# Kernel tuning notes

Measured on AMD Instinct MI355X. Metric: run time of the kernel, lower is better.

Reference implementation:

```python
import jax, jax.numpy as jnp
import numpy as np

B, T, CIN, F, K, U, FF, N, LS = 16, 384, 64, 64, 32, 128, 1024, 64, 15
EPS = 1e-3  # keras BatchNormalization epsilon

def _conv1d(x, w):
    # x:[B,T,C], w:[K,C,F], 'same' padding, no bias
    return jax.lax.conv_general_dilated(x, w, (1,), 'SAME', dimension_numbers=('NWC', 'WIO', 'NWC'))

def _bn(x, g, b, m, v):
    # inference-mode batchnorm
    return g * (x - m) * jax.lax.rsqrt(v + EPS) + b

def _gru_seq(x, k, rk, b):
    # keras GRU (reset_after=True), gate order [z, r, h]; x:[B,T,D] -> [B,T,U]
    u = rk.shape[0]
    xp = x @ k + b[0]                      # precompute input projections [B,T,3U]
    def step(h, xt):
        rec = h @ rk + b[1]
        xz, xr, xh = jnp.split(xt, 3, axis=-1)
        rz, rr_, rh = jnp.split(rec, 3, axis=-1)
        z = jax.nn.sigmoid(xz + rz)
        r = jax.nn.sigmoid(xr + rr_)
        hh = jnp.tanh(xh + r * rh)
        hn = z * h + (1.0 - z) * hh
        return hn, hn
    h0 = jnp.zeros((x.shape[0], u), x.dtype)
    _, ys = jax.lax.scan(step, h0, jnp.swapaxes(xp, 0, 1))
    return jnp.swapaxes(ys, 0, 1)

def _cgru(xr, xi, kr, rkr, br, ki, rki, bi):
    # ComplexGRUCell: real_gru applied to both parts, imag_gru applied to both parts
    rr = _gru_seq(xr, kr, rkr, br)
    ri = _gru_seq(xi, kr, rkr, br)
    ir = _gru_seq(xr, ki, rki, bi)
    ii = _gru_seq(xi, ki, rki, bi)
    return rr - ii, ri + ir

def _forward(h_real, h_imag, conv_wr, conv_wi, bn_gr, bn_br, bn_mr, bn_vr, bn_gi, bn_bi, bn_mi, bn_vi, g0_kr, g0_rkr, g0_br, g0_ki, g0_rki, g0_bi, gs_kr, gs_rkr, gs_br, gs_ki, gs_rki, gs_bi, ff1_w, ff1_b, ff2_w, ff2_b, qr_w, qr_b, qi_w, qi_b, rr_w, rr_b, ri_w, ri_b):
    xr = _bn(_conv1d(h_real, conv_wr) - _conv1d(h_imag, conv_wi), bn_gr, bn_br, bn_mr, bn_vr)
    xi = _bn(_conv1d(h_imag, conv_wr) + _conv1d(h_real, conv_wi), bn_gi, bn_bi, bn_mi, bn_vi)
    xr, xi = _cgru(xr, xi, g0_kr, g0_rkr, g0_br, g0_ki, g0_rki, g0_bi)
    for i in range(LS):  # fixed small layer count
        xr, xi = _cgru(xr, xi, gs_kr[i], gs_rkr[i], gs_br[i], gs_ki[i], gs_rki[i], gs_bi[i])
    def ff(a):
        return jax.nn.relu(a @ ff1_w + ff1_b) @ ff2_w + ff2_b
    xr = xr + ff(xr)   # dropout is identity at inference
    xi = xi + ff(xi)
    mr = jnp.mean(xr, axis=1)
    mi = jnp.mean(xi, axis=1)
    Qr = (mr @ qr_w + qr_b) - (mi @ qi_w + qi_b)
    Qi = (mi @ qr_w + qr_b) + (mr @ qi_w + qi_b)
    Rr = (mr @ rr_w + rr_b) - (mi @ ri_w + ri_b)
    Ri = (mi @ rr_w + rr_b) + (mr @ ri_w + ri_b)
    Qr = Qr.reshape(-1, N, N); Qi = Qi.reshape(-1, N, N)
    Rr = Rr.reshape(-1, N, N); Ri = Ri.reshape(-1, N, N)
    # trace(Q Q^H) = sum |Q|^2 (real, nonnegative)
    nrm = jnp.sqrt(jnp.sum(Qr * Qr + Qi * Qi, axis=(1, 2)))[:, None, None]
    scale = jnp.sqrt(jnp.float32(N)) / nrm
    return Qr * scale, Qi * scale, Rr, Ri

def setup_inputs():
    key = jax.random.key(0)
    ks = jax.random.split(key, 20)
    s = 0.05
    def nrm(k, shape, scale=s):
        return jax.random.normal(k, shape, jnp.float32) * scale
    inp = {}
    inp['h_real'] = nrm(ks[0], (B, T, CIN), 1.0)
    inp['h_imag'] = nrm(ks[1], (B, T, CIN), 1.0)
    inp['conv_wr'] = nrm(ks[2], (K, CIN, F))
    inp['conv_wi'] = nrm(ks[3], (K, CIN, F))
    for nm in ('bn_gr', 'bn_gi', 'bn_vr', 'bn_vi'):
        inp[nm] = jnp.ones((F,), jnp.float32)
    for nm in ('bn_br', 'bn_bi', 'bn_mr', 'bn_mi'):
        inp[nm] = jnp.zeros((F,), jnp.float32)
    inp['g0_kr'] = nrm(ks[4], (F, 3 * U));  inp['g0_rkr'] = nrm(ks[5], (U, 3 * U));  inp['g0_br'] = jnp.zeros((2, 3 * U), jnp.float32)
    inp['g0_ki'] = nrm(ks[6], (F, 3 * U));  inp['g0_rki'] = nrm(ks[7], (U, 3 * U));  inp['g0_bi'] = jnp.zeros((2, 3 * U), jnp.float32)
    inp['gs_kr'] = nrm(ks[8], (LS, U, 3 * U));  inp['gs_rkr'] = nrm(ks[9], (LS, U, 3 * U));  inp['gs_br'] = jnp.zeros((LS, 2, 3 * U), jnp.float32)
    inp['gs_ki'] = nrm(ks[10], (LS, U, 3 * U)); inp['gs_rki'] = nrm(ks[11], (LS, U, 3 * U)); inp['gs_bi'] = jnp.zeros((LS, 2, 3 * U), jnp.float32)
    inp['ff1_w'] = nrm(ks[12], (U, FF)); inp['ff1_b'] = jnp.zeros((FF,), jnp.float32)
    inp['ff2_w'] = nrm(ks[13], (FF, U)); inp['ff2_b'] = jnp.zeros((U,), jnp.float32)
    inp['qr_w'] = nrm(ks[14], (U, N * N)); inp['qr_b'] = jnp.zeros((N * N,), jnp.float32)
    inp['qi_w'] = nrm(ks[15], (U, N * N)); inp['qi_b'] = jnp.zeros((N * N,), jnp.float32)
    inp['rr_w'] = nrm(ks[16], (U, N * N)); inp['rr_b'] = jnp.zeros((N * N,), jnp.float32)
    inp['ri_w'] = nrm(ks[17], (U, N * N)); inp['ri_b'] = jnp.zeros((N * N,), jnp.float32)
    return inp

def reference(h_real, h_imag, conv_wr, conv_wi, bn_gr, bn_br, bn_mr, bn_vr, bn_gi, bn_bi, bn_mi, bn_vi, g0_kr, g0_rkr, g0_br, g0_ki, g0_rki, g0_bi, gs_kr, gs_rkr, gs_br, gs_ki, gs_rki, gs_bi, ff1_w, ff1_b, ff2_w, ff2_b, qr_w, qr_b, qi_w, qi_b, rr_w, rr_b, ri_w, ri_b):
    return _forward(h_real, h_imag, conv_wr, conv_wi, bn_gr, bn_br, bn_mr, bn_vr, bn_gi, bn_bi, bn_mi, bn_vi, g0_kr, g0_rkr, g0_br, g0_ki, g0_rki, g0_bi, gs_kr, gs_rkr, gs_br, gs_ki, gs_rki, gs_bi, ff1_w, ff1_b, ff2_w, ff2_b, qr_w, qr_b, qi_w, qi_b, rr_w, rr_b, ri_w, ri_b)
```

## Files before the change

### kernel.cpp

```cpp
#include <hip/hip_runtime.h>
#include <hip/hip_bf16.h>
#include <math.h>

typedef __attribute__((ext_vector_type(8))) short short8;
typedef __attribute__((ext_vector_type(4))) float f32x4;
typedef unsigned short u16;
typedef unsigned int u32;

#define CL 16
#define NCHUNK 24
#define RING 4
#define CHSZ (16*CL*128)

__device__ __forceinline__ u16 f2bf(float f){
  u32 x = __float_as_uint(f);
  u32 r = x + 0x7fffu + ((x >> 16) & 1u);
  return (u16)(r >> 16);
}
__device__ __forceinline__ float bf2f(u16 u){
  return __uint_as_float(((u32)u) << 16);
}
__device__ __forceinline__ f32x4 mfma16(short8 a, short8 b, f32x4 c){
  return __builtin_amdgcn_mfma_f32_16x16x32_bf16(a, b, c, 0, 0, 0);
}

__global__ void k_init(float* S, float* ssq, u32* Flg){
  int i = blockIdx.x*256 + threadIdx.x;
  if (i < 32768){ S[i] = 0.f; return; }
  i -= 32768;
  if (i < 16){ ssq[i] = 0.f; return; }
  i -= 16;
  if (i < 4096){ Flg[i] = 0u; return; }
}

__global__ void k_wprep(const float* __restrict__ wr, const float* __restrict__ wi,
                        const float* __restrict__ w1,
                        u16* WtR, u16* WtI, u16* WtIN, u16* W1t){
  int i = blockIdx.x*256 + threadIdx.x;
  if (i < 131072){
    int k = i >> 12, r = i & 4095, f = r >> 6, c = r & 63;
    float a = wr[(k<<12) + (c<<6) + f];
    float b = wi[(k<<12) + (c<<6) + f];
    WtR[i] = f2bf(a); WtI[i] = f2bf(b); WtIN[i] = f2bf(-b);
  } else if (i < 262144){
    int j = i - 131072;
    int col = j >> 7, k = j & 127;
    W1t[j] = f2bf(w1[(k<<10) + col]);
  }
}

__global__ __launch_bounds__(256) void k_wprep2(
    const float* __restrict__ g0_kr, const float* __restrict__ g0_ki,
    const float* __restrict__ gs_kr, const float* __restrict__ gs_ki,
    const float* __restrict__ g0_rkr, const float* __restrict__ g0_rki,
    const float* __restrict__ gs_rkr, const float* __restrict__ gs_rki,
    u16* __restrict__ KT, u16* __restrict__ RKT){
  __shared__ float tile[128][33];
  int bid = blockIdx.x;
  int ct = bid % 12; int lm = (bid/12) & 31; int which = bid / (12*32);
  int m = lm & 1, l = lm >> 1;
  int c0 = ct*32;
  int tid = threadIdx.x;
  for (int idx = tid; idx < 128*32; idx += 256){
    int k = idx >> 5, cc = idx & 31;
    float v;
    if (!which){
      if (l == 0) v = (k < 64) ? (m ? g0_ki : g0_kr)[k*384 + c0+cc] : 0.f;
      else        v = (m ? gs_ki : gs_kr)[((size_t)(l-1)*128 + k)*384 + c0+cc];
    } else {
      if (l == 0) v = (m ? g0_rki : g0_rkr)[k*384 + c0+cc];
      else        v = (m ? gs_rki : gs_rkr)[((size_t)(l-1)*128 + k)*384 + c0+cc];
    }
    tile[k][cc] = v;
  }
  __syncthreads();
  u16* dst = (which ? RKT : KT) + (size_t)lm*384*128;
  for (int idx = tid; idx < 32*128; idx += 256){
    int cc = idx >> 7, k = idx & 127;
    dst[(size_t)(c0+cc)*128 + k] = f2bf(tile[k][cc]);
  }
}

__global__ __launch_bounds__(256) void k_conv(
    const float* __restrict__ hr, const float* __restrict__ hi,
    const u16* __restrict__ WtR, const u16* __restrict__ WtI, const u16* __restrict__ WtIN,
    const float* __restrict__ gr, const float* __restrict__ gi,
    const float* __restrict__ vr, const float* __restrict__ vi,
    const float* __restrict__ br, const float* __restrict__ bi,
    const float* __restrict__ mr, const float* __restrict__ mi,
    u16* __restrict__ X0){
  __shared__ u16 xst[2*48*64];
  int tid = threadIdx.x;
  int bid = blockIdx.x;
  int b = bid / 24, t0 = (bid % 24) * 16;
  for (int el = tid; el < 2*47*64; el += 256){
    int part = el / (47*64); int rem = el % (47*64); int row = rem >> 6; int c = rem & 63;
    int tg = t0 + row - 15;
    const float* src = part ? hi : hr;
    float v = (tg >= 0 && tg < 384) ? src[((size_t)b*384 + tg)*64 + c] : 0.f;
    int idx = (part*48 + row)*64 + c;
    int byte = (idx<<1) ^ ((row&7)<<4);
    *(u16*)((char*)xst + byte) = f2bf(v);
  }
  __syncthreads();
  int lane = tid & 63, wid = tid >> 6, lr = lane & 15, lg = lane >> 4;
  f32x4 accr = {0,0,0,0}, acci = {0,0,0,0};
  for (int k = 0; k < 32; ++k){
    int row = lr + k;
    int swz = (row&7)<<4;
    for (int ch = 0; ch < 2; ++ch){
      int c0 = ch*32 + lg*8;
      int idxr = (0*48 + row)*64 + c0;
      int idxi = (1*48 + row)*64 + c0;
      short8 ar = *(const short8*)((const char*)xst + ((idxr<<1) ^ swz));
      short8 ai = *(const short8*)((const char*)xst + ((idxi<<1) ^ swz));
      size_t wb = ((size_t)(k*64 + wid*16 + lr))*64 + c0;
      short8 bwr = *(const short8*)(WtR + wb);
      short8 bwi = *(const short8*)(WtI + wb);
      short8 bwn = *(const short8*)(WtIN + wb);
      accr = mfma16(ar, bwr, accr);
      accr = mfma16(ai, bwn, accr);
      acci = mfma16(ai, bwr, acci);
      acci = mfma16(ar, bwi, acci);
    }
  }
  int f = wid*16 + lr;
  float sr_ = gr[f] * rsqrtf(vr[f] + 1e-3f), or_ = br[f] - mr[f]*sr_;
  float si_ = gi[f] * rsqrtf(vi[f] + 1e-3f), oi_ = bi[f] - mi[f]*si_;
  for (int r = 0; r < 4; ++r){
    int t = t0 + lg*4 + r;
    X0[(((size_t)0*16 + b)*384 + t)*64 + f] = f2bf(accr[r]*sr_ + or_);
    X0[(((size_t)1*16 + b)*384 + t)*64 + f] = f2bf(acci[r]*si_ + oi_);
  }
}

__global__ __launch_bounds__(512,1) void k_scanp(
    const u16* __restrict__ X0, const u16* __restrict__ KT, const u16* __restrict__ RKT,
    const float* __restrict__ g0_br, const float* __restrict__ g0_bi,
    const float* __restrict__ gs_br, const float* __restrict__ gs_bi,
    u16* __restrict__ HC, u16* __restrict__ HS15, u32* Flg)
{
  int bid = blockIdx.x;
  int l = bid >> 2, s = bid & 3;

  __shared__ u16 xs[16*CL*128];
  __shared__ u16 hs2[2*16*128];
  __shared__ float bsh[4][128];

  int tid = threadIdx.x, lane = tid & 63, wv = tid >> 6, lr = lane & 15, lg = lane >> 4;
  int m = s >> 1;

  const float* Bsrc = (l == 0) ? (m ? g0_bi : g0_br)
                               : ((m ? gs_bi : gs_br) + (size_t)(l-1)*768);
  if (tid < 128){
    int j = tid;
    bsh[0][j] = Bsrc[j]       + Bsrc[384 + j];
    bsh[1][j] = Bsrc[128 + j] + Bsrc[384 + 128 + j];
    bsh[2][j] = Bsrc[256 + j];
    bsh[3][j] = Bsrc[384 + 256 + j];
  }
  for (int i = tid; i < 2048; i += 512) ((u32*)hs2)[i] = 0u;

  const u16* Kp  = KT  + (size_t)(l*2 + m)*384*128;
  const u16* RKp = RKT + (size_t)(l*2 + m)*384*128;
  int cz = wv*16 + lr;
  short8 wz[8], wr2[8], whx[4], whr[4];
  #pragma unroll
  for (int ks = 0; ks < 4; ++ks){
    wz[ks]    = *(const short8*)(RKp + (size_t)cz*128 + ks*32 + lg*8);
    wz[4+ks]  = *(const short8*)(Kp  + (size_t)cz*128 + ks*32 + lg*8);
    wr2[ks]   = *(const short8*)(RKp + (size_t)(128+cz)*128 + ks*32 + lg*8);
    wr2[4+ks] = *(const short8*)(Kp  + (size_t)(128+cz)*128 + ks*32 + lg*8);
    whx[ks]   = *(const short8*)(Kp  + (size_t)(256+cz)*128 + ks*32 + lg*8);
    whr[ks]   = *(const short8*)(RKp + (size_t)(256+cz)*128 + ks*32 + lg*8);
  }

  float hreg[4] = {0.f, 0.f, 0.f, 0.f};

  __syncthreads();
  float bz, br_, bhx, bhr;
  {
    int j = wv*16 + lr;
    bz = bsh[0][j]; br_ = bsh[1][j]; bhx = bsh[2][j]; bhr = bsh[3][j];
  }

  u32* prodF = Flg;
  u32* consF = Flg + 2048;
  int sA = (s & 1) ? 1 : 0, sB = (s & 1) ? 2 : 3;
  int pA = (l-1)*4 + sA, pB = (l-1)*4 + sB;
  float sgn = (s & 1) ? 1.f : -1.f;
  int p = s & 1;
  int me = l*4 + s;

  for (int c = 0; c < NCHUNK; ++c){
    int t0 = c * CL;

    if (tid == 0){
      int guard = 0;
      if (l > 0){
        while (__hip_atomic_load(&prodF[pA*32], __ATOMIC_RELAXED, __HIP_MEMORY_SCOPE_AGENT) < (u32)(c+1) ||
               __hip_atomic_load(&prodF[pB*32], __ATOMIC_RELAXED, __HIP_MEMORY_SCOPE_AGENT) < (u32)(c+1)){
          __builtin_amdgcn_s_sleep(1);
          if (++guard > 10000000) break;
        }
      }
      if (l < 15 && c >= RING){
        guard = 0;
        while (__hip_atomic_load(&consF[me*32], __ATOMIC_RELAXED, __HIP_MEMORY_SCOPE_AGENT) < (u32)(2*(c-RING+1))){
          __builtin_amdgcn_s_sleep(1);
          if (++guard > 10000000) break;
        }
      }
    }
    __syncthreads();

    if (l == 0){
      for (int it = 0; it < 8; ++it){
        int g = tid + it*512;
        int k8 = g & 15, ttv = (g>>4) & 15, b = g >> 8;
        short8 v = {0,0,0,0,0,0,0,0};
        if (k8 < 8) v = *(const short8*)(X0 + (((size_t)p*16 + b)*384 + t0 + ttv)*64 + k8*8);
        int byte = (((b*CL + ttv)*128 + k8*8) << 1) ^ ((b&7)<<4);
        *(short8*)((char*)xs + byte) = v;
      }
      __syncthreads();
    } else {
      __builtin_amdgcn_fence(__ATOMIC_ACQUIRE, "agent");
      int slot = c & (RING-1);
      const u16* baseA = HC + ((size_t)pA*RING + slot)*CHSZ;
      const u16* baseB = HC + ((size_t)pB*RING + slot)*CHSZ;
      for (int it = 0; it < 8; ++it){
        int g = tid + it*512;
        int k8 = g & 15, ttv = (g>>4) & 15, b = g >> 8;
        size_t si = ((size_t)b*CL + ttv)*128 + k8*8;
        short8 va = *(const short8*)(baseA + si);
        short8 vb = *(const short8*)(baseB + si);
        short8 o;
        #pragma unroll
        for (int e = 0; e < 8; ++e){
          float f = bf2f((u16)va[e]) + sgn*bf2f((u16)vb[e]);
          o[e] = (short)f2bf(f);
        }
        int byte = (((b*CL + ttv)*128 + k8*8) << 1) ^ ((b&7)<<4);
        *(short8*)((char*)xs + byte) = o;
      }
      __syncthreads();
      if (tid == 0){
        __hip_atomic_fetch_add(&consF[pA*32], 1u, __ATOMIC_RELAXED, __HIP_MEMORY_SCOPE_AGENT);
        __hip_atomic_fetch_add(&consF[pB*32], 1u, __ATOMIC_RELAXED, __HIP_MEMORY_SCOPE_AGENT);
      }
    }

    u16* outp;
    int Tp, tbase;
    if (l < 15){
      outp = HC + ((size_t)me*RING + (c & (RING-1)))*CHSZ;
      Tp = CL; tbase = 0;
    } else {
      outp = HS15 + (size_t)s*16*384*128;
      Tp = 384; tbase = t0;
    }

    for (int q = 0; q < 4; ++q){
      f32x4 xpz[4], xpr[4], xph[4];
      #pragma unroll
      for (int t2 = 0; t2 < 4; ++t2){
        int tt = q*4 + t2;
        short8 ax[4];
        #pragma unroll
        for (int ks = 0; ks < 4; ++ks){
          int xb = (((lr*CL + tt)*128 + ks*32 + lg*8) << 1) ^ ((lr&7)<<4);
          ax[ks] = *(const short8*)((char*)xs + xb);
        }
        f32x4 az  = {bz, bz, bz, bz};
        f32x4 ar  = {br_, br_, br_, br_};
        f32x4 ahx = {bhx, bhx, bhx, bhx};
        #pragma unroll
        for (int ks = 0; ks < 4; ++ks){
          az  = mfma16(ax[ks], wz[4+ks],  az);
          ar  = mfma16(ax[ks], wr2[4+ks], ar);
          ahx = mfma16(ax[ks], whx[ks],   ahx);
        }
        xpz[t2] = az; xpr[t2] = ar; xph[t2] = ahx;
      }
      #pragma unroll
      for (int t2 = 0; t2 < 4; ++t2){
        int tt = q*4 + t2;
        int hp = tt & 1;
        short8 ah[4];
        #pragma unroll
        for (int ks = 0; ks < 4; ++ks){
          int hb = hp*4096 + (((lr*128 + ks*32 + lg*8) << 1) ^ ((lr&7)<<4));
          ah[ks] = *(const short8*)((char*)hs2 + hb);
        }
        f32x4 az  = xpz[t2];
        f32x4 ar  = xpr[t2];
        f32x4 ahr = {bhr, bhr, bhr, bhr};
        #pragma unroll
        for (int ks = 0; ks < 4; ++ks){
          az  = mfma16(ah[ks], wz[ks],  az);
          ar  = mfma16(ah[ks], wr2[ks], ar);
          ahr = mfma16(ah[ks], whr[ks], ahr);
        }
        int j = wv*16 + lr;
        #pragma unroll
        for (int r = 0; r < 4; ++r){
          int b = lg*4 + r;
          float z  = 1.f/(1.f + __expf(-az[r]));
          float rg = 1.f/(1.f + __expf(-ar[r]));
          float pre = xph[t2][r] + rg*ahr[r];
          pre = fminf(fmaxf(pre, -15.f), 15.f);
          float e2 = __expf(2.f*pre);
          float hh = (e2 - 1.f)/(e2 + 1.f);
          float hn = z*hreg[r] + (1.f - z)*hh;
          hreg[r] = hn;
          u16 hb16 = f2bf(hn);
          int byte = ((hp^1)*4096) + ((((b*128 + j) << 1)) ^ ((b&7)<<4));
          *(u16*)((char*)hs2 + byte) = hb16;
          outp[((size_t)b*Tp + tbase + tt)*128 + j] = hb16;
        }
        __syncthreads();
      }
    }

    if (l < 15 && tid == 0){
      __hip_atomic_fetch_add(&prodF[me*32], 1u, __ATOMIC_RELEASE, __HIP_MEMORY_SCOPE_AGENT);
    }
  }
}

__global__ __launch_bounds__(256) void k_ffs(const u16* __restrict__ HS, const u16* __restrict__ W1t,
                                             const float* __restrict__ b1, float* __restrict__ S){
  int bid = blockIdx.x;
  int part = bid / 384; int rem = bid % 384;
  int b = rem / 24; int rem2 = rem % 24;
  int t0 = (rem2 / 4) * 64, c0 = (rem2 % 4) * 256;
  int tid = threadIdx.x, lane = tid & 63, wid = tid >> 6, lr = lane & 15, lg = lane >> 4;
  int sA = part ? 1 : 0, sB = part ? 2 : 3;
  float sgn = part ? 1.f : -1.f;
  short8 af[4][4];
  #pragma unroll
  for (int rt = 0; rt < 4; ++rt)
    #pragma unroll
    for (int ks = 0; ks < 4; ++ks){
      size_t i1 = (((size_t)sA*16 + b)*384 + t0 + rt*16 + lr)*128 + ks*32 + lg*8;
      size_t i2 = (((size_t)sB*16 + b)*384 + t0 + rt*16 + lr)*128 + ks*32 + lg*8;
      short8 va = *(const short8*)(HS + i1);
      short8 vb = *(const short8*)(HS + i2);
      short8 o;
      #pragma unroll
      for (int e = 0; e < 8; ++e){
        float f = bf2f((u16)va[e]) + sgn*bf2f((u16)vb[e]);
        o[e] = (short)f2bf(f);
      }
      af[rt][ks] = o;
    }
  for (int ctl = 0; ctl < 4; ++ctl){
    int col = c0 + wid*64 + ctl*16 + lr;
    short8 bf[4];
    #pragma unroll
    for (int ks = 0; ks < 4; ++ks)
      bf[ks] = *(const short8*)(W1t + (size_t)col*128 + ks*32 + lg*8);
    float bias = b1[col];
    float ssum = 0.f;
    #pragma unroll
    for (int rt = 0; rt < 4; ++rt){
      f32x4 acc = {0,0,0,0};
      #pragma unroll
      for (int ks = 0; ks < 4; ++ks) acc = mfma16(af[rt][ks], bf[ks], acc);
      #pragma unroll
      for (int r = 0; r < 4; ++r) ssum += fmaxf(acc[r] + bias, 0.f);
    }
    ssum += __shfl_xor(ssum, 16, 64);
    ssum += __shfl_xor(ssum, 32, 64);
    if (lg == 0) atomicAdd(&S[((size_t)part*16 + b)*1024 + col], ssum);
  }
}

__global__ void k_mx(const u16* __restrict__ HS, float* __restrict__ Mx){
  int pb = blockIdx.x; int u = threadIdx.x;
  int p = pb >> 4, b = pb & 15;
  int sA = p ? 1 : 0, sB = p ? 2 : 3;
  float sgn = p ? 1.f : -1.f;
  float s = 0.f;
  for (int t = 0; t < 384; ++t){
    float a = bf2f(HS[(((size_t)sA*16 + b)*384 + t)*128 + u]);
    float c = bf2f(HS[(((size_t)sB*16 + b)*384 + t)*128 + u]);
    s += a + sgn*c;
  }
  Mx[pb*128 + u] = s;
}

__global__ void k_comb(const float* __restrict__ S, const float* __restrict__ Mx,
                       const float* __restrict__ w2, const float* __restrict__ b2,
                       float* __restrict__ M){
  int pb = blockIdx.x; int u = threadIdx.x;
  const float* Sp = S + (size_t)pb*1024;
  float acc = 0.f;
  for (int f = 0; f < 1024; ++f) acc += Sp[f] * w2[(size_t)f*128 + u];
  M[pb*128 + u] = Mx[pb*128 + u] * (1.f/384.f) + acc * (1.f/384.f) + b2[u];
}

__global__ __launch_bounds__(256) void k_qr(const float* __restrict__ M,
    const float* __restrict__ qr_w, const float* __restrict__ qr_b,
    const float* __restrict__ qi_w, const float* __restrict__ qi_b,
    const float* __restrict__ rr_w, const float* __restrict__ rr_b,
    const float* __restrict__ ri_w, const float* __restrict__ ri_b,
    float* __restrict__ out, float* __restrict__ ssq){
  __shared__ float smr[128], smi[128];
  int bid = blockIdx.x; int tid = threadIdx.x;
  int b = bid >> 4; int o = (bid & 15)*256 + tid;
  if (tid < 128){ smr[tid] = M[b*128 + tid]; smi[tid] = M[(16 + b)*128 + tid]; }
  __syncthreads();
  float aq=0, bq=0, cq=0, dq=0, ar=0, br2=0, cr=0, dr=0;
  for (int u = 0; u < 128; ++u){
    float mr = smr[u], mi = smi[u];
    float wqr = qr_w[(size_t)u*4096 + o], wqi = qi_w[(size_t)u*4096 + o];
    float wrr = rr_w[(size_t)u*4096 + o], wri = ri_w[(size_t)u*4096 + o];
    aq += mr*wqr;  bq += mi*wqi;  cq += mi*wqr;  dq += mr*wqi;
    ar += mr*wrr;  br2 += mi*wri; cr += mi*wrr;  dr += mr*wri;
  }
  float Qr = (aq + qr_b[o]) - (bq + qi_b[o]);
  float Qi = (cq + qr_b[o]) + (dq + qi_b[o]);
  float Rr = (ar + rr_b[o]) - (br2 + ri_b[o]);
  float Ri = (cr + rr_b[o]) + (dr + ri_b[o]);
  out[(size_t)b*4096 + o] = Qr;
  out[65536 + (size_t)b*4096 + o] = Qi;
  out[131072 + (size_t)b*4096 + o] = Rr;
  out[196608 + (size_t)b*4096 + o] = Ri;
  float ss = Qr*Qr + Qi*Qi;
  for (int off = 32; off; off >>= 1) ss += __shfl_down(ss, off, 64);
  if ((tid & 63) == 0) atomicAdd(&ssq[b], ss);
}

__global__ void k_scale(float* __restrict__ out, const float* __restrict__ ssq){
  int i = blockIdx.x*256 + threadIdx.x;
  int b = (i >> 12) & 15;
  float s = 8.f / sqrtf(ssq[b]);
  out[i] *= s;
}

extern "C" void kernel_launch(void* const* d_in, const int* in_sizes, int n_in,
                              void* d_out, int out_size, void* d_ws, size_t ws_size,
                              hipStream_t stream){
  const float* h_real = (const float*)d_in[0];
  const float* h_imag = (const float*)d_in[1];
  const float* conv_wr = (const float*)d_in[2];
  const float* conv_wi = (const float*)d_in[3];
  const float* bn_gr = (const float*)d_in[4];
  const float* bn_gi = (const float*)d_in[5];
  const float* bn_vr = (const float*)d_in[6];
  const float* bn_vi = (const float*)d_in[7];
  const float* bn_br = (const float*)d_in[8];
  const float* bn_bi = (const float*)d_in[9];
  const float* bn_mr = (const float*)d_in[10];
  const float* bn_mi = (const float*)d_in[11];
  const float* g0_kr = (const float*)d_in[12];
  const float* g0_rkr = (const float*)d_in[13];
  const float* g0_br = (const float*)d_in[14];
  const float* g0_ki = (const float*)d_in[15];
  const float* g0_rki = (const float*)d_in[16];
  const float* g0_bi = (const float*)d_in[17];
  const float* gs_kr = (const float*)d_in[18];
  const float* gs_rkr = (const float*)d_in[19];
  const float* gs_br = (const float*)d_in[20];
  const float* gs_ki = (const float*)d_in[21];
  const float* gs_rki = (const float*)d_in[22];
  const float* gs_bi = (const float*)d_in[23];
  const float* ff1_w = (const float*)d_in[24];
  const float* ff1_b = (const float*)d_in[25];
  const float* ff2_w = (const float*)d_in[26];
  const float* ff2_b = (const float*)d_in[27];
  const float* qr_w = (const float*)d_in[28];
  const float* qr_b = (const float*)d_in[29];
  const float* qi_w = (const float*)d_in[30];
  const float* qi_b = (const float*)d_in[31];
  const float* rr_w = (const float*)d_in[32];
  const float* rr_b = (const float*)d_in[33];
  const float* ri_w = (const float*)d_in[34];
  const float* ri_b = (const float*)d_in[35];

  char* ws = (char*)d_ws; size_t off = 0;
  auto carve = [&](size_t bytes)->char*{ char* p = ws + off; off += (bytes + 255) & ~(size_t)255; return p; };
  u16* X0   = (u16*)carve((size_t)2*16*384*64*2);
  u16* HC   = (u16*)carve((size_t)64*RING*CHSZ*2);
  u16* HS15 = (u16*)carve((size_t)4*16*384*128*2);
  u16* KT   = (u16*)carve((size_t)16*2*384*128*2);
  u16* RKT  = (u16*)carve((size_t)16*2*384*128*2);
  u16* WtR  = (u16*)carve(131072*2);
  u16* WtI  = (u16*)carve(131072*2);
  u16* WtIN = (u16*)carve(131072*2);
  u16* W1t  = (u16*)carve(131072*2);
  u32* Flg  = (u32*)carve(4096*4);
  float* S  = (float*)carve(32768*4);
  float* Mx = (float*)carve(4096*4);
  float* M  = (float*)carve(4096*4);
  float* ssq = (float*)carve(256);

  k_init<<<145, 256, 0, stream>>>(S, ssq, Flg);
  k_wprep<<<1024, 256, 0, stream>>>(conv_wr, conv_wi, ff1_w, WtR, WtI, WtIN, W1t);
  k_wprep2<<<768, 256, 0, stream>>>(g0_kr, g0_ki, gs_kr, gs_ki,
                                    g0_rkr, g0_rki, gs_rkr, gs_rki, KT, RKT);
  k_conv<<<384, 256, 0, stream>>>(h_real, h_imag, WtR, WtI, WtIN,
                                  bn_gr, bn_gi, bn_vr, bn_vi, bn_br, bn_bi, bn_mr, bn_mi, X0);
  k_scanp<<<64, 512, 0, stream>>>(X0, KT, RKT, g0_br, g0_bi, gs_br, gs_bi,
                                  HC, HS15, Flg);
  k_ffs<<<768, 256, 0, stream>>>(HS15, W1t, ff1_b, S);
  k_mx<<<32, 128, 0, stream>>>(HS15, Mx);
  k_comb<<<32, 128, 0, stream>>>(S, Mx, ff2_w, ff2_b, M);
  k_qr<<<256, 256, 0, stream>>>(M, qr_w, qr_b, qi_w, qi_b, rr_w, rr_b, ri_w, ri_b,
                                (float*)d_out, ssq);
  k_scale<<<512, 256, 0, stream>>>((float*)d_out, ssq);
}
```

Measured before the change: 1.128 ms.

## Double conv time tile per block and split mean reduction across more blocks

```diff
diff --git a/kernel.cpp b/kernel.cpp
--- a/kernel.cpp
+++ b/kernel.cpp
@@ -24,13 +24,15 @@
   return __builtin_amdgcn_mfma_f32_16x16x32_bf16(a, b, c, 0, 0, 0);
 }
 
-__global__ void k_init(float* S, float* ssq, u32* Flg){
+__global__ void k_init(float* S, float* ssq, u32* Flg, float* Mx){
   int i = blockIdx.x*256 + threadIdx.x;
   if (i < 32768){ S[i] = 0.f; return; }
   i -= 32768;
   if (i < 16){ ssq[i] = 0.f; return; }
   i -= 16;
   if (i < 4096){ Flg[i] = 0u; return; }
+  i -= 4096;
+  if (i < 4096){ Mx[i] = 0.f; return; }
 }
 
 __global__ void k_wprep(const float* __restrict__ wr, const float* __restrict__ wi,
@@ -89,48 +91,61 @@
     const float* __restrict__ br, const float* __restrict__ bi,
     const float* __restrict__ mr, const float* __restrict__ mi,
     u16* __restrict__ X0){
-  __shared__ u16 xst[2*48*64];
+  __shared__ u16 xst[2*64*64];
   int tid = threadIdx.x;
   int bid = blockIdx.x;
-  int b = bid / 24, t0 = (bid % 24) * 16;
-  for (int el = tid; el < 2*47*64; el += 256){
-    int part = el / (47*64); int rem = el % (47*64); int row = rem >> 6; int c = rem & 63;
+  int b = bid / 12, t0 = (bid % 12) * 32;
+  for (int el = tid; el < 2*63*64; el += 256){
+    int part = el / (63*64); int rem = el % (63*64); int row = rem >> 6; int c = rem & 63;
     int tg = t0 + row - 15;
     const float* src = part ? hi : hr;
     float v = (tg >= 0 && tg < 384) ? src[((size_t)b*384 + tg)*64 + c] : 0.f;
-    int idx = (part*48 + row)*64 + c;
+    int idx = (part*64 + row)*64 + c;
     int byte = (idx<<1) ^ ((row&7)<<4);
     *(u16*)((char*)xst + byte) = f2bf(v);
   }
   __syncthreads();
   int lane = tid & 63, wid = tid >> 6, lr = lane & 15, lg = lane >> 4;
   f32x4 accr = {0,0,0,0}, acci = {0,0,0,0};
+  f32x4 accr2 = {0,0,0,0}, acci2 = {0,0,0,0};
   for (int k = 0; k < 32; ++k){
     int row = lr + k;
-    int swz = (row&7)<<4;
+    int row2 = row + 16;
+    int swz = (row&7)<<4, swz2 = (row2&7)<<4;
     for (int ch = 0; ch < 2; ++ch){
       int c0 = ch*32 + lg*8;
-      int idxr = (0*48 + row)*64 + c0;
-      int idxi = (1*48 + row)*64 + c0;
-      short8 ar = *(const short8*)((const char*)xst + ((idxr<<1) ^ swz));
-      short8 ai = *(const short8*)((const char*)xst + ((idxi<<1) ^ swz));
+      int idxr  = (0*64 + row )*64 + c0;
+      int idxi  = (1*64 + row )*64 + c0;
+      int idxr2 = (0*64 + row2)*64 + c0;
+      int idxi2 = (1*64 + row2)*64 + c0;
+      short8 ar  = *(const short8*)((const char*)xst + ((idxr <<1) ^ swz));
+      short8 ai  = *(const short8*)((const char*)xst + ((idxi <<1) ^ swz));
+      short8 ar2 = *(const short8*)((const char*)xst + ((idxr2<<1) ^ swz2));
+      short8 ai2 = *(const short8*)((const char*)xst + ((idxi2<<1) ^ swz2));
       size_t wb = ((size_t)(k*64 + wid*16 + lr))*64 + c0;
       short8 bwr = *(const short8*)(WtR + wb);
       short8 bwi = *(const short8*)(WtI + wb);
       short8 bwn = *(const short8*)(WtIN + wb);
-      accr = mfma16(ar, bwr, accr);
-      accr = mfma16(ai, bwn, accr);
-      acci = mfma16(ai, bwr, acci);
-      acci = mfma16(ar, bwi, acci);
+      accr  = mfma16(ar,  bwr, accr);
+      accr  = mfma16(ai,  bwn, accr);
+      acci  = mfma16(ai,  bwr, acci);
+      acci  = mfma16(ar,  bwi, acci);
+      accr2 = mfma16(ar2, bwr, accr2);
+      accr2 = mfma16(ai2, bwn, accr2);
+      acci2 = mfma16(ai2, bwr, acci2);
+      acci2 = mfma16(ar2, bwi, acci2);
     }
   }
   int f = wid*16 + lr;
   float sr_ = gr[f] * rsqrtf(vr[f] + 1e-3f), or_ = br[f] - mr[f]*sr_;
   float si_ = gi[f] * rsqrtf(vi[f] + 1e-3f), oi_ = bi[f] - mi[f]*si_;
   for (int r = 0; r < 4; ++r){
-    int t = t0 + lg*4 + r;
-    X0[(((size_t)0*16 + b)*384 + t)*64 + f] = f2bf(accr[r]*sr_ + or_);
-    X0[(((size_t)1*16 + b)*384 + t)*64 + f] = f2bf(acci[r]*si_ + oi_);
+    int t  = t0 + lg*4 + r;
+    int t2 = t0 + 16 + lg*4 + r;
+    X0[(((size_t)0*16 + b)*384 + t )*64 + f] = f2bf(accr[r] *sr_ + or_);
+    X0[(((size_t)1*16 + b)*384 + t )*64 + f] = f2bf(acci[r] *si_ + oi_);
+    X0[(((size_t)0*16 + b)*384 + t2)*64 + f] = f2bf(accr2[r]*sr_ + or_);
+    X0[(((size_t)1*16 + b)*384 + t2)*64 + f] = f2bf(acci2[r]*si_ + oi_);
   }
 }
 
@@ -194,6 +209,7 @@
 
   for (int c = 0; c < NCHUNK; ++c){
     int t0 = c * CL;
+    int slot = c & (RING-1);
 
     if (tid == 0){
       int guard = 0;
@@ -226,7 +242,6 @@
       __syncthreads();
     } else {
       __builtin_amdgcn_fence(__ATOMIC_ACQUIRE, "agent");
-      int slot = c & (RING-1);
       const u16* baseA = HC + ((size_t)pA*RING + slot)*CHSZ;
       const u16* baseB = HC + ((size_t)pB*RING + slot)*CHSZ;
       for (int it = 0; it < 8; ++it){
@@ -254,7 +269,7 @@
     u16* outp;
     int Tp, tbase;
     if (l < 15){
-      outp = HC + ((size_t)me*RING + (c & (RING-1)))*CHSZ;
+      outp = HC + ((size_t)me*RING + slot)*CHSZ;
       Tp = CL; tbase = 0;
     } else {
       outp = HS15 + (size_t)s*16*384*128;
@@ -378,17 +393,18 @@
 }
 
 __global__ void k_mx(const u16* __restrict__ HS, float* __restrict__ Mx){
-  int pb = blockIdx.x; int u = threadIdx.x;
+  int bid = blockIdx.x; int u = threadIdx.x;
+  int pb = bid >> 2, tq = bid & 3;
   int p = pb >> 4, b = pb & 15;
   int sA = p ? 1 : 0, sB = p ? 2 : 3;
   float sgn = p ? 1.f : -1.f;
   float s = 0.f;
-  for (int t = 0; t < 384; ++t){
+  for (int t = tq*96; t < tq*96 + 96; ++t){
     float a = bf2f(HS[(((size_t)sA*16 + b)*384 + t)*128 + u]);
     float c = bf2f(HS[(((size_t)sB*16 + b)*384 + t)*128 + u]);
     s += a + sgn*c;
   }
-  Mx[pb*128 + u] = s;
+  atomicAdd(&Mx[pb*128 + u], s);
 }
 
 __global__ void k_comb(const float* __restrict__ S, const float* __restrict__ Mx,
@@ -497,16 +513,16 @@
   float* M  = (float*)carve(4096*4);
   float* ssq = (float*)carve(256);
 
-  k_init<<<145, 256, 0, stream>>>(S, ssq, Flg);
+  k_init<<<161, 256, 0, stream>>>(S, ssq, Flg, Mx);
   k_wprep<<<1024, 256, 0, stream>>>(conv_wr, conv_wi, ff1_w, WtR, WtI, WtIN, W1t);
   k_wprep2<<<768, 256, 0, stream>>>(g0_kr, g0_ki, gs_kr, gs_ki,
                                     g0_rkr, g0_rki, gs_rkr, gs_rki, KT, RKT);
-  k_conv<<<384, 256, 0, stream>>>(h_real, h_imag, WtR, WtI, WtIN,
+  k_conv<<<192, 256, 0, stream>>>(h_real, h_imag, WtR, WtI, WtIN,
                                   bn_gr, bn_gi, bn_vr, bn_vi, bn_br, bn_bi, bn_mr, bn_mi, X0);
   k_scanp<<<64, 512, 0, stream>>>(X0, KT, RKT, g0_br, g0_bi, gs_br, gs_bi,
                                   HC, HS15, Flg);
   k_ffs<<<768, 256, 0, stream>>>(HS15, W1t, ff1_b, S);
-  k_mx<<<32, 128, 0, stream>>>(HS15, Mx);
+  k_mx<<<128, 128, 0, stream>>>(HS15, Mx);
   k_comb<<<32, 128, 0, stream>>>(S, Mx, ff2_w, ff2_b, M);
   k_qr<<<256, 256, 0, stream>>>(M, qr_w, qr_b, qi_w, qi_b, rr_w, rr_b, ri_w, ri_b,
                                 (float*)d_out, ssq);
```

After: 1.093 ms. 1.03x faster.
